# Kernel tuning notes

Hardware: AMD Instinct MI355X
Metric: run time of the kernel (lower is better)

Reference implementation:

```python
import jax, jax.numpy as jnp
import numpy as np

N, C, L = 64, 3, 4096
K, S = 128, 64  # num_shapelets, shapelets_size


def setup_inputs() -> dict:
    key = jax.random.key(0)
    kx, ks = jax.random.split(key)
    x = jax.random.normal(kx, (N, C, L), dtype=jnp.float32)
    shapelets = jax.random.normal(ks, (C, K, S), dtype=jnp.float32)
    return {"x": x, "shapelets": shapelets}


def _min_euclid(x, shapelets):
    # x: (N, C, L); shapelets: (C, K, S)
    # Torch does unfold -> cdist -> min over windows -> min over channels.
    # We compute ||x_w - s||^2 = ||x_w||^2 + ||s||^2 - 2<x_w, s> with sliding
    # dot products via grouped 1-D conv (avoids materializing the unfold).
    C_, K_, S_ = shapelets.shape
    n = x.shape[0]
    filt = shapelets.reshape(C_ * K_, 1, S_)  # OIW, grouped by channel
    dots = jax.lax.conv_general_dilated(
        x, filt, window_strides=(1,), padding="VALID",
        dimension_numbers=("NCW", "OIW", "NCW"),
        feature_group_count=C_)                      # (N, C*K, W)
    ones = jnp.ones((C_, 1, S_), x.dtype)
    x2 = jax.lax.conv_general_dilated(
        x * x, ones, window_strides=(1,), padding="VALID",
        dimension_numbers=("NCW", "OIW", "NCW"),
        feature_group_count=C_)                      # (N, C, W) sliding ||x_w||^2
    W_ = dots.shape[-1]
    dots = dots.reshape(n, C_, K_, W_)               # (N, C, K, W)
    s2 = jnp.sum(shapelets * shapelets, axis=-1)     # (C, K)
    d2 = x2[:, :, None, :] + s2[None, :, :, None] - 2.0 * dots
    d = jnp.sqrt(jnp.maximum(d2, 0.0))               # Euclidean distance (N,C,K,W)
    d = jnp.min(d, axis=3)                           # min over windows -> (N, C, K)
    d = jnp.min(d, axis=1)                           # min over channels -> (N, K)
    return d[:, None, :]                             # (N, 1, K)


def reference(x, shapelets):
    return _min_euclid(x, shapelets)
```

## Files before the change

### kernel.cpp

```cpp
#include <hip/hip_runtime.h>
#include <hip/hip_bf16.h>

#define NN 64
#define CC 3
#define LL 4096
#define SS 64
#define KK 128
#define WW 4033
#define TILES 32
#define TPB 4
#define BLKN (TILES/TPB)

typedef __attribute__((ext_vector_type(8))) short v8s;
typedef __attribute__((ext_vector_type(4))) float v4f;

#define WS_CNT_OFF 32768
#define WS_HS2_OFF 33024
#define WS_SHB_OFF 34560

__device__ __forceinline__ unsigned bf16_rne(float f) {
    unsigned u = __float_as_uint(f);
    return (u + 0x7FFFu + ((u >> 16) & 1u)) >> 16;
}

__global__ void me_prep(const float* __restrict__ shp,
                        unsigned* __restrict__ d2g,
                        unsigned* __restrict__ cnt,
                        float* __restrict__ hs2g,
                        uint4* __restrict__ shb) {
    int tid = blockIdx.x * 256 + threadIdx.x;
    if (tid < NN * KK) d2g[tid] = 0x7F800000u;
    if (tid < NN) cnt[tid] = 0u;
    if (tid < CC * KK) {
        const float* r = shp + tid * SS;
        float a = 0.f;
        #pragma unroll 8
        for (int s = 0; s < SS; ++s) a += r[s] * r[s];
        hs2g[tid] = -0.5f * a;
    }
    if (tid < CC * 1024) {
        int c  = tid >> 10;
        int r  = tid & 1023;
        int nt = r >> 7;
        int sc = (r >> 6) & 1;
        int l  = r & 63;
        int row  = nt * 16 + (l & 15);
        int koff = sc * 32 + (l >> 4) * 8;
        const float* s = shp + ((size_t)(c * KK + row)) * SS + koff;
        float4 f0 = *(const float4*)s;
        float4 f1 = *(const float4*)(s + 4);
        uint4 o;
        o.x = (bf16_rne(f0.y) << 16) | bf16_rne(f0.x);
        o.y = (bf16_rne(f0.w) << 16) | bf16_rne(f0.z);
        o.z = (bf16_rne(f1.y) << 16) | bf16_rne(f1.x);
        o.w = (bf16_rne(f1.w) << 16) | bf16_rne(f1.z);
        shb[tid] = o;
    }
}

__global__ __launch_bounds__(256, 2) void me_main(
        const float* __restrict__ x,
        const ushort* __restrict__ shb_g,
        const float* __restrict__ hs2g,
        unsigned* __restrict__ d2g,
        unsigned* __restrict__ cnt,
        float* __restrict__ out) {

    __shared__ __align__(16) ushort shb[CC * 8192];
    __shared__ ushort xs2[2][2][CC][200];
    __shared__ __align__(16) float hx2s[2][CC][128];
    __shared__ unsigned red[KK];
    __shared__ int lastflag;

    const int b    = blockIdx.x;
    const int n    = b >> 3;
    const int tg   = b & 7;
    const int t    = threadIdx.x;
    const int lane = t & 63, wave = t >> 6;
    const int quad = lane >> 4, col = lane & 15;
    const int wbase = wave * 32;

    if (t < KK) red[t] = 0x7F800000u;

    {
        typedef __attribute__((address_space(1))) const uint4 gu4;
        typedef __attribute__((address_space(3))) uint4 lu4;
        const uint4* gbase = (const uint4*)shb_g;
        #pragma unroll
        for (int it = 0; it < 12; ++it) {
            const uint4* gp = gbase + it * 256 + t;
            uint4* lp = (uint4*)shb + (it * 256 + wave * 64);
            __builtin_amdgcn_global_load_lds((gu4*)gp, (lu4*)lp, 16, 0, 0);
        }
    }

    float hsv[CC][8];
    #pragma unroll
    for (int c = 0; c < CC; ++c)
        #pragma unroll
        for (int nt = 0; nt < 8; ++nt)
            hsv[c][nt] = hs2g[c * KK + nt * 16 + col];

    const float* xb = x + (size_t)n * (CC * LL);

    float rmax[8];
    #pragma unroll
    for (int nt = 0; nt < 8; ++nt) rmax[nt] = -3.4e38f;

    for (int j = 0; j < TPB; ++j) {
        const int buf = j & 1;
        const int w0  = (tg * TPB + j) * 128;

        if (wave < 3) {
            const float* xc = xb + wave * LL;
            float P0, P1, P2;
            float carry = 0.f;
            #pragma unroll
            for (int seg = 0; seg < 3; ++seg) {
                int idx = seg * 64 + lane;
                int gi  = w0 + idx;
                float v = (gi < LL) ? xc[gi] : 0.f;
                ushort hv = (ushort)bf16_rne(v);
                xs2[buf][0][wave][idx] = hv;
                if (idx > 0) xs2[buf][1][wave][idx - 1] = hv;
                float sq = v * v;
                #pragma unroll
                for (int d = 1; d < 64; d <<= 1) {
                    float u = __shfl_up(sq, d, 64);
                    if (lane >= d) sq += u;
                }
                sq += carry;
                if (seg == 0) P0 = sq; else if (seg == 1) P1 = sq; else P2 = sq;
                carry = __shfl(sq, 63, 64);
            }
            float p0u = __shfl_up(P0, 1, 64);
            float p1u = __shfl_up(P1, 1, 64);
            float p2u = __shfl_up(P2, 1, 64);
            float P0e = __shfl(P0, 63, 64);
            float P1e = __shfl(P1, 63, 64);
            float I1a = (lane == 0) ? P0e : p1u;
            float I0a = (lane == 0) ? 0.f : p0u;
            float I1b = (lane == 0) ? P1e : p2u;
            hx2s[buf][wave][lane]      = (w0 + lane < WW)      ? (-0.5f * (I1a - I0a)) : -1e30f;
            hx2s[buf][wave][64 + lane] = (w0 + 64 + lane < WW) ? (-0.5f * (I1b - I1a)) : -1e30f;
        }
        __syncthreads();

        #pragma unroll
        for (int c = 0; c < CC; ++c) {
            v4f hxv[2];
            #pragma unroll
            for (int mt = 0; mt < 2; ++mt)
                hxv[mt] = *(const v4f*)(&hx2s[buf][c][wbase + mt * 16 + quad * 4]);
            v8s af[2][2];
            #pragma unroll
            for (int mt = 0; mt < 2; ++mt)
                #pragma unroll
                for (int sc = 0; sc < 2; ++sc) {
                    int e0 = wbase + mt * 16 + col + sc * 32 + quad * 8;
                    int p  = col & 1;
                    const uint* ap = (const uint*)&xs2[buf][p][c][e0 - p];
                    union { v8s v; uint u[4]; } au;
                    au.u[0] = ap[0]; au.u[1] = ap[1];
                    au.u[2] = ap[2]; au.u[3] = ap[3];
                    af[mt][sc] = au.v;
                }
            v4f acc[8][2];
            #pragma unroll
            for (int nt = 0; nt < 8; ++nt) {
                float h = hsv[c][nt];
                #pragma unroll
                for (int mt = 0; mt < 2; ++mt) {
                    v4f a;
                    a[0] = hxv[mt][0] + h; a[1] = hxv[mt][1] + h;
                    a[2] = hxv[mt][2] + h; a[3] = hxv[mt][3] + h;
                    acc[nt][mt] = a;
                }
            }
            #pragma unroll
            for (int sc = 0; sc < 2; ++sc)
                #pragma unroll
                for (int nt = 0; nt < 8; ++nt) {
                    v8s bfr = *(const v8s*)(shb + (((c * 8 + nt) * 2 + sc) * 64 + lane) * 8);
                    acc[nt][0] = __builtin_amdgcn_mfma_f32_16x16x32_bf16(af[0][sc], bfr, acc[nt][0], 0, 0, 0);
                    acc[nt][1] = __builtin_amdgcn_mfma_f32_16x16x32_bf16(af[1][sc], bfr, acc[nt][1], 0, 0, 0);
                }
            #pragma unroll
            for (int nt = 0; nt < 8; ++nt) {
                v4f a0 = acc[nt][0], a1 = acc[nt][1];
                float m = fmaxf(fmaxf(fmaxf(a0[0], a0[1]), fmaxf(a0[2], a0[3])),
                                fmaxf(fmaxf(a1[0], a1[1]), fmaxf(a1[2], a1[3])));
                rmax[nt] = fmaxf(rmax[nt], m);
            }
        }
    }

    #pragma unroll
    for (int nt = 0; nt < 8; ++nt) {
        float v = rmax[nt];
        v = fmaxf(v, __shfl_xor(v, 16, 64));
        v = fmaxf(v, __shfl_xor(v, 32, 64));
        rmax[nt] = v;
    }
    if (quad == 0) {
        #pragma unroll
        for (int nt = 0; nt < 8; ++nt) {
            float d2 = fmaxf(-2.f * rmax[nt], 0.f);
            atomicMin(&red[nt * 16 + col], __float_as_uint(d2));
        }
    }
    __syncthreads();
    if (t < KK) atomicMin(&d2g[n * KK + t], red[t]);

    __syncthreads();
    if (t == 0) {
        unsigned old = atomicAdd(&cnt[n], 1u);
        lastflag = (old == BLKN - 1) ? 1 : 0;
    }
    __syncthreads();
    if (lastflag && t < KK) {
        unsigned bits = atomicMin(&d2g[n * KK + t], 0x7F800000u);
        out[n * KK + t] = sqrtf(__uint_as_float(bits));
    }
}

extern "C" void kernel_launch(void* const* d_in, const int* in_sizes, int n_in,
                              void* d_out, int out_size, void* d_ws, size_t ws_size,
                              hipStream_t stream) {
    const float* x   = (const float*)d_in[0];
    const float* shp = (const float*)d_in[1];
    unsigned* d2g  = (unsigned*)d_ws;
    unsigned* cnt  = (unsigned*)((char*)d_ws + WS_CNT_OFF);
    float*    hs2g = (float*)((char*)d_ws + WS_HS2_OFF);
    uint4*    shb  = (uint4*)((char*)d_ws + WS_SHB_OFF);
    float* out = (float*)d_out;

    hipLaunchKernelGGL(me_prep, dim3(32), dim3(256), 0, stream, shp, d2g, cnt, hs2g, shb);
    hipLaunchKernelGGL(me_main, dim3(NN * TILES / TPB), dim3(256), 0, stream,
                       x, (const ushort*)shb, hs2g, d2g, cnt, out);
}
```

Measured before the change: 80.50 us.

## Precompute sliding window sq-norms in prep kernel and add them after MFMA

Moves the sliding-window ||x_w||^2 prefix-sum computation out of the main kernel into extra prep blocks. Each prep block scans one full (n,c) row and writes per-window half-norms to workspace. The main kernel now only converts x to bf16 in LDS using all threads, then reads the norms from global memory. The norm is added after the MFMA accumulation instead of being used to seed the accumulator. This removes serial shuffle scans and wave imbalance from the main loop, at the cost of an extra global write and read of a roughly 3 MB buffer plus more prep blocks.

After: 79.40 us. About the same (-1.4%).

```diff
diff --git a/kernel.cpp b/kernel.cpp
--- a/kernel.cpp
+++ b/kernel.cpp
@@ -17,44 +17,101 @@
 #define WS_CNT_OFF 32768
 #define WS_HS2_OFF 33024
 #define WS_SHB_OFF 34560
+#define WS_HX2_OFF 131072
 
 __device__ __forceinline__ unsigned bf16_rne(float f) {
     unsigned u = __float_as_uint(f);
     return (u + 0x7FFFu + ((u >> 16) & 1u)) >> 16;
 }
 
-__global__ void me_prep(const float* __restrict__ shp,
-                        unsigned* __restrict__ d2g,
-                        unsigned* __restrict__ cnt,
-                        float* __restrict__ hs2g,
-                        uint4* __restrict__ shb) {
-    int tid = blockIdx.x * 256 + threadIdx.x;
-    if (tid < NN * KK) d2g[tid] = 0x7F800000u;
-    if (tid < NN) cnt[tid] = 0u;
-    if (tid < CC * KK) {
-        const float* r = shp + tid * SS;
-        float a = 0.f;
-        #pragma unroll 8
-        for (int s = 0; s < SS; ++s) a += r[s] * r[s];
-        hs2g[tid] = -0.5f * a;
-    }
-    if (tid < CC * 1024) {
-        int c  = tid >> 10;
-        int r  = tid & 1023;
-        int nt = r >> 7;
-        int sc = (r >> 6) & 1;
-        int l  = r & 63;
-        int row  = nt * 16 + (l & 15);
-        int koff = sc * 32 + (l >> 4) * 8;
-        const float* s = shp + ((size_t)(c * KK + row)) * SS + koff;
-        float4 f0 = *(const float4*)s;
-        float4 f1 = *(const float4*)(s + 4);
-        uint4 o;
-        o.x = (bf16_rne(f0.y) << 16) | bf16_rne(f0.x);
-        o.y = (bf16_rne(f0.w) << 16) | bf16_rne(f0.z);
-        o.z = (bf16_rne(f1.y) << 16) | bf16_rne(f1.x);
-        o.w = (bf16_rne(f1.w) << 16) | bf16_rne(f1.z);
-        shb[tid] = o;
+__global__ __launch_bounds__(256) void me_prep(
+        const float* __restrict__ x,
+        const float* __restrict__ shp,
+        unsigned* __restrict__ d2g,
+        unsigned* __restrict__ cnt,
+        float* __restrict__ hs2g,
+        uint4* __restrict__ shb,
+        float* __restrict__ hx2g) {
+    const int b = blockIdx.x, t = threadIdx.x;
+    if (b < NN * CC) {
+        const int n = b / 3, c = b - n * 3;
+        __shared__ float P[LL];
+        __shared__ float wtot[4];
+        const int lane = t & 63, wave = t >> 6;
+        const float* xc = x + ((size_t)n * CC + c) * LL;
+        const int base = t * 16;
+        float q[16];
+        {
+            float4 A0 = *(const float4*)(xc + base);
+            float4 A1 = *(const float4*)(xc + base + 4);
+            float4 A2 = *(const float4*)(xc + base + 8);
+            float4 A3 = *(const float4*)(xc + base + 12);
+            q[0]=A0.x; q[1]=A0.y; q[2]=A0.z;  q[3]=A0.w;
+            q[4]=A1.x; q[5]=A1.y; q[6]=A1.z;  q[7]=A1.w;
+            q[8]=A2.x; q[9]=A2.y; q[10]=A2.z; q[11]=A2.w;
+            q[12]=A3.x;q[13]=A3.y;q[14]=A3.z; q[15]=A3.w;
+        }
+        float run = 0.f;
+        #pragma unroll
+        for (int i = 0; i < 16; ++i) { run += q[i] * q[i]; q[i] = run; }
+        float sc = run;
+        #pragma unroll
+        for (int d = 1; d < 64; d <<= 1) {
+            float u = __shfl_up(sc, d, 64);
+            if (lane >= d) sc += u;
+        }
+        if (lane == 63) wtot[wave] = sc;
+        __syncthreads();
+        float excl = sc - run;
+        for (int w2 = 0; w2 < wave; ++w2) excl += wtot[w2];
+        #pragma unroll
+        for (int i = 0; i < 16; ++i) q[i] += excl;
+        *(float4*)(P + base)      = make_float4(q[0], q[1], q[2], q[3]);
+        *(float4*)(P + base + 4)  = make_float4(q[4], q[5], q[6], q[7]);
+        *(float4*)(P + base + 8)  = make_float4(q[8], q[9], q[10], q[11]);
+        *(float4*)(P + base + 12) = make_float4(q[12], q[13], q[14], q[15]);
+        __syncthreads();
+        float* dst = hx2g + ((size_t)n * CC + c) * LL;
+        #pragma unroll
+        for (int i = 0; i < 16; ++i) {
+            int w = base + i;
+            float o = -1e30f;
+            if (w < WW) {
+                float I1 = P[w + 63];
+                float I0 = (w > 0) ? P[w - 1] : 0.f;
+                o = -0.5f * (I1 - I0);
+            }
+            dst[w] = o;
+        }
+    } else {
+        int tid = (b - NN * CC) * 256 + t;
+        if (tid < NN * KK) d2g[tid] = 0x7F800000u;
+        if (tid < NN) cnt[tid] = 0u;
+        if (tid < CC * KK) {
+            const float* r = shp + tid * SS;
+            float a = 0.f;
+            #pragma unroll 8
+            for (int s = 0; s < SS; ++s) a += r[s] * r[s];
+            hs2g[tid] = -0.5f * a;
+        }
+        if (tid < CC * 1024) {
+            int c  = tid >> 10;
+            int r  = tid & 1023;
+            int nt = r >> 7;
+            int scb = (r >> 6) & 1;
+            int l  = r & 63;
+            int row  = nt * 16 + (l & 15);
+            int koff = scb * 32 + (l >> 4) * 8;
+            const float* s = shp + ((size_t)(c * KK + row)) * SS + koff;
+            float4 f0 = *(const float4*)s;
+            float4 f1 = *(const float4*)(s + 4);
+            uint4 o;
+            o.x = (bf16_rne(f0.y) << 16) | bf16_rne(f0.x);
+            o.y = (bf16_rne(f0.w) << 16) | bf16_rne(f0.z);
+            o.z = (bf16_rne(f1.y) << 16) | bf16_rne(f1.x);
+            o.w = (bf16_rne(f1.w) << 16) | bf16_rne(f1.z);
+            shb[tid] = o;
+        }
     }
 }
 
@@ -62,13 +119,13 @@
         const float* __restrict__ x,
         const ushort* __restrict__ shb_g,
         const float* __restrict__ hs2g,
+        const float* __restrict__ hx2g,
         unsigned* __restrict__ d2g,
         unsigned* __restrict__ cnt,
         float* __restrict__ out) {
 
     __shared__ __align__(16) ushort shb[CC * 8192];
     __shared__ ushort xs2[2][2][CC][200];
-    __shared__ __align__(16) float hx2s[2][CC][128];
     __shared__ unsigned red[KK];
     __shared__ int lastflag;
 
@@ -101,7 +158,8 @@
         for (int nt = 0; nt < 8; ++nt)
             hsv[c][nt] = hs2g[c * KK + nt * 16 + col];
 
-    const float* xb = x + (size_t)n * (CC * LL);
+    const float* xb   = x + (size_t)n * (CC * LL);
+    const float* hx2b = hx2g + (size_t)n * (CC * LL);
 
     float rmax[8];
     #pragma unroll
@@ -111,47 +169,25 @@
         const int buf = j & 1;
         const int w0  = (tg * TPB + j) * 128;
 
-        if (wave < 3) {
-            const float* xc = xb + wave * LL;
-            float P0, P1, P2;
-            float carry = 0.f;
-            #pragma unroll
-            for (int seg = 0; seg < 3; ++seg) {
-                int idx = seg * 64 + lane;
-                int gi  = w0 + idx;
-                float v = (gi < LL) ? xc[gi] : 0.f;
-                ushort hv = (ushort)bf16_rne(v);
-                xs2[buf][0][wave][idx] = hv;
-                if (idx > 0) xs2[buf][1][wave][idx - 1] = hv;
-                float sq = v * v;
-                #pragma unroll
-                for (int d = 1; d < 64; d <<= 1) {
-                    float u = __shfl_up(sq, d, 64);
-                    if (lane >= d) sq += u;
-                }
-                sq += carry;
-                if (seg == 0) P0 = sq; else if (seg == 1) P1 = sq; else P2 = sq;
-                carry = __shfl(sq, 63, 64);
-            }
-            float p0u = __shfl_up(P0, 1, 64);
-            float p1u = __shfl_up(P1, 1, 64);
-            float p2u = __shfl_up(P2, 1, 64);
-            float P0e = __shfl(P0, 63, 64);
-            float P1e = __shfl(P1, 63, 64);
-            float I1a = (lane == 0) ? P0e : p1u;
-            float I0a = (lane == 0) ? 0.f : p0u;
-            float I1b = (lane == 0) ? P1e : p2u;
-            hx2s[buf][wave][lane]      = (w0 + lane < WW)      ? (-0.5f * (I1a - I0a)) : -1e30f;
-            hx2s[buf][wave][64 + lane] = (w0 + 64 + lane < WW) ? (-0.5f * (I1b - I1a)) : -1e30f;
+        #pragma unroll
+        for (int it = 0; it < 3; ++it) {
+            int e = t + it * 256;
+            if (e < 576) {
+                int c = e / 192, idx = e - c * 192;
+                int gi = w0 + idx;
+                float vx = (gi < LL) ? xb[c * LL + gi] : 0.f;
+                ushort hv = (ushort)bf16_rne(vx);
+                xs2[buf][0][c][idx] = hv;
+                if (idx > 0) xs2[buf][1][c][idx - 1] = hv;
+            }
         }
         __syncthreads();
 
         #pragma unroll
         for (int c = 0; c < CC; ++c) {
-            v4f hxv[2];
-            #pragma unroll
-            for (int mt = 0; mt < 2; ++mt)
-                hxv[mt] = *(const v4f*)(&hx2s[buf][c][wbase + mt * 16 + quad * 4]);
+            const float* hp = hx2b + c * LL + w0 + wbase + quad * 4;
+            v4f hxv0 = *(const v4f*)(hp);
+            v4f hxv1 = *(const v4f*)(hp + 16);
             v8s af[2][2];
             #pragma unroll
             for (int mt = 0; mt < 2; ++mt)
@@ -169,13 +205,8 @@
             #pragma unroll
             for (int nt = 0; nt < 8; ++nt) {
                 float h = hsv[c][nt];
-                #pragma unroll
-                for (int mt = 0; mt < 2; ++mt) {
-                    v4f a;
-                    a[0] = hxv[mt][0] + h; a[1] = hxv[mt][1] + h;
-                    a[2] = hxv[mt][2] + h; a[3] = hxv[mt][3] + h;
-                    acc[nt][mt] = a;
-                }
+                v4f a = {h, h, h, h};
+                acc[nt][0] = a; acc[nt][1] = a;
             }
             #pragma unroll
             for (int sc = 0; sc < 2; ++sc)
@@ -188,8 +219,10 @@
             #pragma unroll
             for (int nt = 0; nt < 8; ++nt) {
                 v4f a0 = acc[nt][0], a1 = acc[nt][1];
-                float m = fmaxf(fmaxf(fmaxf(a0[0], a0[1]), fmaxf(a0[2], a0[3])),
-                                fmaxf(fmaxf(a1[0], a1[1]), fmaxf(a1[2], a1[3])));
+                float m = -3.4e38f;
+                #pragma unroll
+                for (int r = 0; r < 4; ++r)
+                    m = fmaxf(m, fmaxf(a0[r] + hxv0[r], a1[r] + hxv1[r]));
                 rmax[nt] = fmaxf(rmax[nt], m);
             }
         }
@@ -233,9 +266,11 @@
     unsigned* cnt  = (unsigned*)((char*)d_ws + WS_CNT_OFF);
     float*    hs2g = (float*)((char*)d_ws + WS_HS2_OFF);
     uint4*    shb  = (uint4*)((char*)d_ws + WS_SHB_OFF);
+    float*    hx2g = (float*)((char*)d_ws + WS_HX2_OFF);
     float* out = (float*)d_out;
 
-    hipLaunchKernelGGL(me_prep, dim3(32), dim3(256), 0, stream, shp, d2g, cnt, hs2g, shb);
+    hipLaunchKernelGGL(me_prep, dim3(NN * CC + 32), dim3(256), 0, stream,
+                       x, shp, d2g, cnt, hs2g, shb, hx2g);
     hipLaunchKernelGGL(me_main, dim3(NN * TILES / TPB), dim3(256), 0, stream,
-                       x, (const ushort*)shb, hs2g, d2g, cnt, out);
-}
+                       x, (const ushort*)shb, hs2g, hx2g, d2g, cnt, out);
+}
```

## Process full 512-window tile per block and convert shapelets to bf16 in-kernel

Applied to the files above, without the earlier changes.

Each block now handles its whole 512-window span in one pass instead of four 128-window iterations. Each wave covers 128 windows (8 M-tiles) and loops over groups of 2 shapelet tiles, so B fragments are reused across 8 MFMAs. The window norm is applied after the MFMA instead of being folded into the accumulator init. Shapelet bf16 packing moves from the prep kernel into the main kernel, so every block converts from fp32 global memory instead of doing an async global-to-LDS copy. The prep kernel shrinks to an init-only launch. Risks are higher register pressure from the 8x2 fragment arrays and redundant shapelet conversion work in every block.

Result: faster. 77.68 us (-3.5%).

```diff
diff --git a/kernel.cpp b/kernel.cpp
--- a/kernel.cpp
+++ b/kernel.cpp
@@ -7,29 +7,27 @@
 #define SS 64
 #define KK 128
 #define WW 4033
-#define TILES 32
-#define TPB 4
-#define BLKN (TILES/TPB)
+#define BLKN 8
 
 typedef __attribute__((ext_vector_type(8))) short v8s;
 typedef __attribute__((ext_vector_type(4))) float v4f;
 
 #define WS_CNT_OFF 32768
 #define WS_HS2_OFF 33024
-#define WS_SHB_OFF 34560
 
 __device__ __forceinline__ unsigned bf16_rne(float f) {
     unsigned u = __float_as_uint(f);
     return (u + 0x7FFFu + ((u >> 16) & 1u)) >> 16;
 }
 
-__global__ void me_prep(const float* __restrict__ shp,
-                        unsigned* __restrict__ d2g,
-                        unsigned* __restrict__ cnt,
-                        float* __restrict__ hs2g,
-                        uint4* __restrict__ shb) {
+__global__ __launch_bounds__(256) void me_init(
+        const float* __restrict__ shp,
+        unsigned* __restrict__ d2g,
+        unsigned* __restrict__ cnt,
+        float* __restrict__ hs2g) {
     int tid = blockIdx.x * 256 + threadIdx.x;
-    if (tid < NN * KK) d2g[tid] = 0x7F800000u;
+    uint4 inf4 = {0x7F800000u, 0x7F800000u, 0x7F800000u, 0x7F800000u};
+    ((uint4*)d2g)[tid] = inf4;
     if (tid < NN) cnt[tid] = 0u;
     if (tid < CC * KK) {
         const float* r = shp + tid * SS;
@@ -38,15 +36,45 @@
         for (int s = 0; s < SS; ++s) a += r[s] * r[s];
         hs2g[tid] = -0.5f * a;
     }
-    if (tid < CC * 1024) {
-        int c  = tid >> 10;
-        int r  = tid & 1023;
-        int nt = r >> 7;
-        int sc = (r >> 6) & 1;
-        int l  = r & 63;
+}
+
+__global__ __launch_bounds__(256, 2) void me_main(
+        const float* __restrict__ x,
+        const float* __restrict__ shp,
+        const float* __restrict__ hs2g,
+        unsigned* __restrict__ d2g,
+        unsigned* __restrict__ cnt,
+        float* __restrict__ out) {
+
+    __shared__ __align__(16) ushort shb[CC * 8192];
+    __shared__ __align__(8) ushort xs2[2][CC][640];
+    __shared__ float Pp[CC][580];
+    __shared__ float hx2s[CC][512];
+    __shared__ unsigned red[KK];
+    __shared__ int lastflag;
+
+    const int b    = blockIdx.x;
+    const int n    = b >> 3;
+    const int tg   = b & 7;
+    const int w0   = tg * 512;
+    const int t    = threadIdx.x;
+    const int lane = t & 63, wave = t >> 6;
+    const int quad = lane >> 4, col = lane & 15;
+    const int wbase = wave * 128;
+
+    if (t < KK) red[t] = 0x7F800000u;
+
+    #pragma unroll
+    for (int it = 0; it < 12; ++it) {
+        int cidx = t + it * 256;
+        int c   = cidx >> 10;
+        int r   = cidx & 1023;
+        int nt  = r >> 7;
+        int scb = (r >> 6) & 1;
+        int l   = r & 63;
         int row  = nt * 16 + (l & 15);
-        int koff = sc * 32 + (l >> 4) * 8;
-        const float* s = shp + ((size_t)(c * KK + row)) * SS + koff;
+        int koff = scb * 32 + (l >> 4) * 8;
+        const float* s = shp + (size_t)(c * KK + row) * SS + koff;
         float4 f0 = *(const float4*)s;
         float4 f1 = *(const float4*)(s + 4);
         uint4 o;
@@ -54,44 +82,7 @@
         o.y = (bf16_rne(f0.w) << 16) | bf16_rne(f0.z);
         o.z = (bf16_rne(f1.y) << 16) | bf16_rne(f1.x);
         o.w = (bf16_rne(f1.w) << 16) | bf16_rne(f1.z);
-        shb[tid] = o;
-    }
-}
-
-__global__ __launch_bounds__(256, 2) void me_main(
-        const float* __restrict__ x,
-        const ushort* __restrict__ shb_g,
-        const float* __restrict__ hs2g,
-        unsigned* __restrict__ d2g,
-        unsigned* __restrict__ cnt,
-        float* __restrict__ out) {
-
-    __shared__ __align__(16) ushort shb[CC * 8192];
-    __shared__ ushort xs2[2][2][CC][200];
-    __shared__ __align__(16) float hx2s[2][CC][128];
-    __shared__ unsigned red[KK];
-    __shared__ int lastflag;
-
-    const int b    = blockIdx.x;
-    const int n    = b >> 3;
-    const int tg   = b & 7;
-    const int t    = threadIdx.x;
-    const int lane = t & 63, wave = t >> 6;
-    const int quad = lane >> 4, col = lane & 15;
-    const int wbase = wave * 32;
-
-    if (t < KK) red[t] = 0x7F800000u;
-
-    {
-        typedef __attribute__((address_space(1))) const uint4 gu4;
-        typedef __attribute__((address_space(3))) uint4 lu4;
-        const uint4* gbase = (const uint4*)shb_g;
-        #pragma unroll
-        for (int it = 0; it < 12; ++it) {
-            const uint4* gp = gbase + it * 256 + t;
-            uint4* lp = (uint4*)shb + (it * 256 + wave * 64);
-            __builtin_amdgcn_global_load_lds((gu4*)gp, (lu4*)lp, 16, 0, 0);
-        }
+        ((uint4*)shb)[cidx] = o;
     }
 
     float hsv[CC][8];
@@ -103,94 +94,95 @@
 
     const float* xb = x + (size_t)n * (CC * LL);
 
+    if (wave < 3) {
+        const float* xc = xb + wave * LL;
+        float carry = 0.f;
+        #pragma unroll
+        for (int seg = 0; seg < 9; ++seg) {
+            int idx = seg * 64 + lane;
+            int gi  = w0 + idx;
+            float v = (gi < LL) ? xc[gi] : 0.f;
+            ushort hv = (ushort)bf16_rne(v);
+            xs2[0][wave][idx] = hv;
+            if (idx > 0) xs2[1][wave][idx - 1] = hv;
+            float sq = v * v;
+            #pragma unroll
+            for (int d = 1; d < 64; d <<= 1) {
+                float u = __shfl_up(sq, d, 64);
+                if (lane >= d) sq += u;
+            }
+            sq += carry;
+            Pp[wave][idx] = sq;
+            carry = __shfl(sq, 63, 64);
+        }
+    }
+    __syncthreads();
+
+    #pragma unroll
+    for (int it = 0; it < 6; ++it) {
+        int e = t + it * 256;
+        int c = e >> 9, w = e & 511;
+        float I1 = Pp[c][w + 63];
+        float I0 = (w > 0) ? Pp[c][w - 1] : 0.f;
+        hx2s[c][w] = (w0 + w < WW) ? (-0.5f * (I1 - I0)) : -1e30f;
+    }
+    __syncthreads();
+
     float rmax[8];
     #pragma unroll
     for (int nt = 0; nt < 8; ++nt) rmax[nt] = -3.4e38f;
 
-    for (int j = 0; j < TPB; ++j) {
-        const int buf = j & 1;
-        const int w0  = (tg * TPB + j) * 128;
-
-        if (wave < 3) {
-            const float* xc = xb + wave * LL;
-            float P0, P1, P2;
-            float carry = 0.f;
-            #pragma unroll
-            for (int seg = 0; seg < 3; ++seg) {
-                int idx = seg * 64 + lane;
-                int gi  = w0 + idx;
-                float v = (gi < LL) ? xc[gi] : 0.f;
-                ushort hv = (ushort)bf16_rne(v);
-                xs2[buf][0][wave][idx] = hv;
-                if (idx > 0) xs2[buf][1][wave][idx - 1] = hv;
-                float sq = v * v;
+    #pragma unroll
+    for (int c = 0; c < CC; ++c) {
+        v4f hxv[8];
+        #pragma unroll
+        for (int mt = 0; mt < 8; ++mt)
+            hxv[mt] = *(const v4f*)(&hx2s[c][wbase + mt * 16 + quad * 4]);
+        v8s af[8][2];
+        #pragma unroll
+        for (int mt = 0; mt < 8; ++mt)
+            #pragma unroll
+            for (int sc = 0; sc < 2; ++sc) {
+                int e0 = wbase + mt * 16 + col + sc * 32 + quad * 8;
+                int p  = col & 1;
+                const uint* ap = (const uint*)&xs2[p][c][e0 - p];
+                union { v8s v; uint u[4]; } au;
+                au.u[0] = ap[0]; au.u[1] = ap[1];
+                au.u[2] = ap[2]; au.u[3] = ap[3];
+                af[mt][sc] = au.v;
+            }
+        #pragma unroll
+        for (int g = 0; g < 4; ++g) {
+            v4f acc[2][8];
+            #pragma unroll
+            for (int nt2 = 0; nt2 < 2; ++nt2) {
+                float h = hsv[c][g * 2 + nt2];
+                v4f a = {h, h, h, h};
                 #pragma unroll
-                for (int d = 1; d < 64; d <<= 1) {
-                    float u = __shfl_up(sq, d, 64);
-                    if (lane >= d) sq += u;
-                }
-                sq += carry;
-                if (seg == 0) P0 = sq; else if (seg == 1) P1 = sq; else P2 = sq;
-                carry = __shfl(sq, 63, 64);
-            }
-            float p0u = __shfl_up(P0, 1, 64);
-            float p1u = __shfl_up(P1, 1, 64);
-            float p2u = __shfl_up(P2, 1, 64);
-            float P0e = __shfl(P0, 63, 64);
-            float P1e = __shfl(P1, 63, 64);
-            float I1a = (lane == 0) ? P0e : p1u;
-            float I0a = (lane == 0) ? 0.f : p0u;
-            float I1b = (lane == 0) ? P1e : p2u;
-            hx2s[buf][wave][lane]      = (w0 + lane < WW)      ? (-0.5f * (I1a - I0a)) : -1e30f;
-            hx2s[buf][wave][64 + lane] = (w0 + 64 + lane < WW) ? (-0.5f * (I1b - I1a)) : -1e30f;
-        }
-        __syncthreads();
-
-        #pragma unroll
-        for (int c = 0; c < CC; ++c) {
-            v4f hxv[2];
-            #pragma unroll
-            for (int mt = 0; mt < 2; ++mt)
-                hxv[mt] = *(const v4f*)(&hx2s[buf][c][wbase + mt * 16 + quad * 4]);
-            v8s af[2][2];
-            #pragma unroll
-            for (int mt = 0; mt < 2; ++mt)
-                #pragma unroll
-                for (int sc = 0; sc < 2; ++sc) {
-                    int e0 = wbase + mt * 16 + col + sc * 32 + quad * 8;
-                    int p  = col & 1;
-                    const uint* ap = (const uint*)&xs2[buf][p][c][e0 - p];
-                    union { v8s v; uint u[4]; } au;
-                    au.u[0] = ap[0]; au.u[1] = ap[1];
-                    au.u[2] = ap[2]; au.u[3] = ap[3];
-                    af[mt][sc] = au.v;
-                }
-            v4f acc[8][2];
-            #pragma unroll
-            for (int nt = 0; nt < 8; ++nt) {
-                float h = hsv[c][nt];
-                #pragma unroll
-                for (int mt = 0; mt < 2; ++mt) {
-                    v4f a;
-                    a[0] = hxv[mt][0] + h; a[1] = hxv[mt][1] + h;
-                    a[2] = hxv[mt][2] + h; a[3] = hxv[mt][3] + h;
-                    acc[nt][mt] = a;
-                }
+                for (int mt = 0; mt < 8; ++mt) acc[nt2][mt] = a;
             }
             #pragma unroll
             for (int sc = 0; sc < 2; ++sc)
                 #pragma unroll
-                for (int nt = 0; nt < 8; ++nt) {
+                for (int nt2 = 0; nt2 < 2; ++nt2) {
+                    int nt = g * 2 + nt2;
                     v8s bfr = *(const v8s*)(shb + (((c * 8 + nt) * 2 + sc) * 64 + lane) * 8);
-                    acc[nt][0] = __builtin_amdgcn_mfma_f32_16x16x32_bf16(af[0][sc], bfr, acc[nt][0], 0, 0, 0);
-                    acc[nt][1] = __builtin_amdgcn_mfma_f32_16x16x32_bf16(af[1][sc], bfr, acc[nt][1], 0, 0, 0);
+                    #pragma unroll
+                    for (int mt = 0; mt < 8; ++mt)
+                        acc[nt2][mt] = __builtin_amdgcn_mfma_f32_16x16x32_bf16(
+                            af[mt][sc], bfr, acc[nt2][mt], 0, 0, 0);
                 }
             #pragma unroll
-            for (int nt = 0; nt < 8; ++nt) {
-                v4f a0 = acc[nt][0], a1 = acc[nt][1];
-                float m = fmaxf(fmaxf(fmaxf(a0[0], a0[1]), fmaxf(a0[2], a0[3])),
-                                fmaxf(fmaxf(a1[0], a1[1]), fmaxf(a1[2], a1[3])));
-                rmax[nt] = fmaxf(rmax[nt], m);
+            for (int nt2 = 0; nt2 < 2; ++nt2) {
+                float m = -3.4e38f;
+                #pragma unroll
+                for (int mt = 0; mt < 8; ++mt) {
+                    v4f a = acc[nt2][mt];
+                    #pragma unroll
+                    for (int r = 0; r < 4; ++r)
+                        m = fmaxf(m, a[r] + hxv[mt][r]);
+                }
+                rmax[g * 2 + nt2] = fmaxf(rmax[g * 2 + nt2], m);
             }
         }
     }
@@ -232,10 +224,9 @@
     unsigned* d2g  = (unsigned*)d_ws;
     unsigned* cnt  = (unsigned*)((char*)d_ws + WS_CNT_OFF);
     float*    hs2g = (float*)((char*)d_ws + WS_HS2_OFF);
-    uint4*    shb  = (uint4*)((char*)d_ws + WS_SHB_OFF);
     float* out = (float*)d_out;
 
-    hipLaunchKernelGGL(me_prep, dim3(32), dim3(256), 0, stream, shp, d2g, cnt, hs2g, shb);
-    hipLaunchKernelGGL(me_main, dim3(NN * TILES / TPB), dim3(256), 0, stream,
-                       x, (const ushort*)shb, hs2g, d2g, cnt, out);
-}
+    hipLaunchKernelGGL(me_init, dim3(8), dim3(256), 0, stream, shp, d2g, cnt, hs2g);
+    hipLaunchKernelGGL(me_main, dim3(NN * BLKN), dim3(256), 0, stream,
+                       x, shp, hs2g, d2g, cnt, out);
+}
```
